# Performance work log

Hardware: AMD Instinct MI355X
Metric: run time of the kernel (lower is better)

The kernel has to match this reference:

```python
import jax, jax.numpy as jnp
from jax import lax
import numpy as np

B, T, D = 16, 750, 2048
C = 20            # num_classes
H = 8             # num heads (CMA on feat_dim = D//2 = 1024)
DH = (D // 2) // H
R_EASY, R_HARD, SM, SB = 5, 20, 3, 6  # r_easy, r_hard, m, M
EPS = 1e-12


def setup_inputs() -> dict:
    key = jax.random.key(0)
    ks = jax.random.split(key, 8)
    d2 = D // 2
    return {
        'x': jax.random.normal(ks[0], (B, T, D), jnp.float32),
        'rgb_proj': jax.random.normal(ks[1], (H, d2, DH), jnp.float32) * 0.03,
        'flow_proj': jax.random.normal(ks[2], (H, d2, DH), jnp.float32) * 0.03,
        'atte_w': jax.random.normal(ks[3], (H, DH, DH), jnp.float32) * 0.09,
        'embed_w': jax.random.normal(ks[4], (2048, D, 9), jnp.float32) * 0.02,
        'embed_b': jnp.zeros((2048,), jnp.float32),
        'cls1_w': jax.random.normal(ks[5], (C, 2048, 9), jnp.float32) * 0.02,
        'cls2_w': jax.random.normal(ks[6], (C, 1, 7), jnp.float32) * 0.1,
    }


def _l2norm(v):
    # torch F.normalize: v / max(||v||, eps)
    n = jnp.sqrt(jnp.sum(v * v, axis=-1, keepdims=True))
    return v / jnp.maximum(n, EPS)


def _conv1d(x, w, pad, dil=1, groups=1):
    # x: (N, Cin, L), w: (Cout, Cin/groups, K)
    return lax.conv_general_dilated(x, w, (1,), [(pad, pad)], rhs_dilation=(dil,),
                                    dimension_numbers=('NCH', 'OIH', 'NCH'),
                                    feature_group_count=groups)


def _erode(b, w):
    # scipy binary_erosion, structure ones((1,w)), border_value=0
    left = w // 2
    bp = jnp.pad(b, ((0, 0), (left, w - 1 - left)))
    return lax.reduce_window(bp, jnp.inf, lax.min, (1, w), (1, 1), 'VALID')


def _dilate(b, w):
    # scipy binary_dilation (reflected structure), border_value=0
    right = w // 2
    bp = jnp.pad(b, ((0, 0), (w - 1 - right, right)))
    return lax.reduce_window(bp, -jnp.inf, lax.max, (1, w), (1, 1), 'VALID')


def _topk_gather(scores, emb, k):
    _, idx = lax.top_k(scores, k)           # (N, k), descending like torch.sort
    return jnp.take_along_axis(emb, idx[:, :, None], axis=1)


def reference(x, rgb_proj, flow_proj, atte_w, embed_w, embed_b, cls1_w, cls2_w):
    n, l, _ = x.shape
    k_easy, k_hard = l // R_EASY, l // R_HARD
    rgb, flow = x[..., :D // 2], x[..., D // 2:]

    # ---- CMA cross-modal attention ----
    o_rgb = _l2norm(jnp.einsum('nld,hde->nhle', rgb, rgb_proj))    # (n,H,l,dh)
    o_flow = _l2norm(jnp.einsum('nld,hde->nhle', flow, flow_proj))
    atte = jnp.einsum('nhlf,nhmf->nhlm', jnp.einsum('nhle,hef->nhlf', o_rgb, atte_w), o_flow)
    rgb_atte = jax.nn.softmax(atte, axis=-1)
    flow_atte = jax.nn.softmax(jnp.swapaxes(atte, -1, -2), axis=-1)
    e_rgb = jax.nn.gelu(jnp.einsum('nhlm,nhme->nhle', rgb_atte, o_rgb), approximate=False)
    e_flow = jax.nn.gelu(jnp.einsum('nhlm,nhme->nhle', flow_atte, o_flow), approximate=False)
    f_rgb = jnp.tanh(jnp.swapaxes(e_rgb, 1, 2).reshape(n, l, -1) + rgb)
    f_flow = jnp.tanh(jnp.swapaxes(e_flow, 1, 2).reshape(n, l, -1) + flow)
    xc = jnp.concatenate([f_rgb, f_flow], axis=-1)                 # (n,l,D)

    # ---- Actionness module (eval mode: dropouts are identity) ----
    xt = jnp.swapaxes(xc, 1, 2)                                    # (n,D,l)
    emb = jax.nn.relu(_conv1d(xt, embed_w, pad=4) + embed_b[None, :, None])
    embeddings = jnp.swapaxes(emb, 1, 2)                           # (n,l,2048)
    o = _conv1d(emb, cls1_w, pad=4)                                # (n,C,l)
    o = jax.nn.relu(_conv1d(o, cls2_w, pad=6, dil=2, groups=C))
    cas = jnp.swapaxes(o, 1, 2)                                    # (n,l,C)
    actionness = jnp.sum(cas, axis=2)                              # (n,l)

    # ---- easy snippet mining ----
    easy_act = _topk_gather(actionness, embeddings, k_easy)
    a_rev = jnp.max(actionness, axis=1, keepdims=True) - actionness
    easy_bkg = _topk_gather(a_rev, embeddings, k_easy)

    # ---- hard snippet mining (median threshold + 1D morphology) ----
    med = jnp.median(actionness, axis=1, keepdims=True)
    abin = jnp.where(actionness > med, 1.0, 0.0).astype(actionness.dtype)
    inner = actionness * (_erode(abin, SM) - _erode(abin, SB))
    hard_act = _topk_gather(inner, embeddings, k_hard)
    outer = actionness * (_dilate(abin, SB) - _dilate(abin, SM))
    hard_bkg = _topk_gather(outer, embeddings, k_hard)

    # ---- video class scores ----
    top_cas, _ = lax.top_k(jnp.swapaxes(cas, 1, 2), k_easy)        # (n,C,k)
    video_scores = jax.nn.softmax(jnp.mean(top_cas, axis=-1), axis=1)
    return (video_scores, easy_act, easy_bkg, hard_act, hard_bkg, actionness, cas)
```

## Files before the change

### kernel.cpp

```cpp
#include <hip/hip_runtime.h>
#include <cstdio>
#include <cstdint>

typedef __bf16 bf16;
typedef __attribute__((ext_vector_type(8))) __bf16 bf16x8;
typedef __attribute__((ext_vector_type(4))) __bf16 bf16x4;
typedef __attribute__((ext_vector_type(4))) float f32x4;
typedef unsigned long long u64;
typedef unsigned int u32;

constexpr int BATCH = 16, TT = 750, DD = 2048, NC = 20;
constexpr int MM = 12000;
constexpr int PT = 758;
constexpr int PCH = 32;
constexpr int NCHUNK = 4;
constexpr int RPC = 3000;
constexpr int SROW = 752;
constexpr int SPAIR = 750 * SROW;
constexpr int KE = 150, KH = 37;

constexpr size_t OUT_EA  = 320;
constexpr size_t OUT_EB  = OUT_EA + (size_t)BATCH * KE * DD;
constexpr size_t OUT_HA  = OUT_EB + (size_t)BATCH * KE * DD;
constexpr size_t OUT_HB  = OUT_HA + (size_t)BATCH * KH * DD;
constexpr size_t OUT_ACT = OUT_HB + (size_t)BATCH * KH * DD;
constexpr size_t OUT_CAS = OUT_ACT + MM;

constexpr size_t XCB = (size_t)(BATCH * PT) * DD * 2;
constexpr size_t O_XC1   = 0;
constexpr size_t O_XC2   = O_XC1 + XCB;
constexpr size_t O_XC3   = O_XC2 + XCB;
constexpr size_t O_EM1   = O_XC3 + XCB;
constexpr size_t O_EM2   = O_EM1 + XCB;
constexpr size_t O_EM3   = O_EM2 + XCB;
constexpr size_t O_CAS1  = O_EM3 + XCB;
constexpr size_t O_CAST  = O_CAS1 + 960000;
constexpr size_t O_ACT   = O_CAST + 960000;
constexpr size_t O_AREV  = O_ACT + 48000;
constexpr size_t O_INNER = O_AREV + 48000;
constexpr size_t O_OUTER = O_INNER + 48000;
constexpr size_t O_SMEAN = O_OUTER + 48000;
constexpr size_t O_IDX   = O_SMEAN + 1280;
constexpr size_t O_RSINV = O_IDX + 23936;
constexpr size_t O_CSINV = O_RSINV + 96000;
constexpr size_t O_DBG   = O_CSINV + 96000;
constexpr size_t AR      = O_DBG + 256;

constexpr size_t SB   = (size_t)PCH * SPAIR * 4;
constexpr size_t PL   = (size_t)PCH * 750 * 128 * 2;
constexpr size_t TPL  = (size_t)PCH * 128 * 768 * 2;
constexpr size_t O_S    = AR;
constexpr size_t O_ST   = O_S + SB;
constexpr size_t O_Q1   = O_ST + SB;
constexpr size_t O_Q2   = O_Q1 + PL;
constexpr size_t O_Q3   = O_Q2 + PL;
constexpr size_t O_OR1  = O_Q3 + PL;
constexpr size_t O_OR2  = O_OR1 + PL;
constexpr size_t O_OR3  = O_OR2 + PL;
constexpr size_t O_OF1  = O_OR3 + PL;
constexpr size_t O_OF2  = O_OF1 + PL;
constexpr size_t O_OF3  = O_OF2 + PL;
constexpr size_t O_OTR1 = O_OF3 + PL;
constexpr size_t O_OTR2 = O_OTR1 + TPL;
constexpr size_t O_OTR3 = O_OTR2 + TPL;
constexpr size_t O_OTF1 = O_OTR3 + TPL;
constexpr size_t O_OTF2 = O_OTF1 + TPL;
constexpr size_t O_OTF3 = O_OTF2 + TPL;
constexpr size_t O_OPRE = O_OTF3 + TPL;
constexpr size_t PRP  = (size_t)1024 * 1024 * 2;
constexpr size_t O_PR1  = O_OPRE + (size_t)RPC * 1024 * 4;
constexpr size_t O_PR2  = O_PR1 + PRP;
constexpr size_t O_PR3  = O_PR2 + PRP;
constexpr size_t O_PF1  = O_PR3 + PRP;
constexpr size_t O_PF2  = O_PF1 + PRP;
constexpr size_t O_PF3  = O_PF2 + PRP;
constexpr size_t AWP  = (size_t)8 * 128 * 128 * 2;
constexpr size_t O_AW1  = O_PF3 + PRP;
constexpr size_t O_AW2  = O_AW1 + AWP;
constexpr size_t O_AW3  = O_AW2 + AWP;
constexpr size_t WS_NEED = O_AW3 + AWP;

constexpr size_t WTP  = (size_t)9 * 2048 * 2048 * 2;
constexpr size_t O_WT1  = AR;
constexpr size_t O_WT2  = O_WT1 + WTP;
constexpr size_t O_WT3  = O_WT2 + WTP;
constexpr size_t WCP  = (size_t)9 * 32 * 2048 * 2;
constexpr size_t O_WC1  = O_WT3 + WTP;
constexpr size_t O_WC2  = O_WC1 + WCP;
constexpr size_t O_WC3  = O_WC2 + WCP;

static_assert(O_WC3 + WCP <= WS_NEED, "WT/WC overrun");
static_assert(WS_NEED <= 603979776, "exceeds harness ws");

struct bf3 { bf16 h, m, l; };
static __device__ __forceinline__ bf3 split3(float v) {
  bf3 r;
  r.h = (bf16)v;
  float rem = v - (float)r.h;
  r.m = (bf16)rem;
  r.l = (bf16)(rem - (float)r.m);
  return r;
}
static __device__ __forceinline__ bf16x8 bzero8() {
  bf16x8 v;
#pragma unroll
  for (int i = 0; i < 8; i++) v[i] = (bf16)0.f;
  return v;
}
static __device__ __forceinline__ u32 asc_enc(float f) {
  u32 u = __float_as_uint(f);
  return (u & 0x80000000u) ? ~u : (u | 0x80000000u);
}
static __device__ __forceinline__ float asc_dec(u32 a) {
  u32 u = (a & 0x80000000u) ? (a ^ 0x80000000u) : ~a;
  return __uint_as_float(u);
}
static __device__ void bsort1024(u64* ks) {
  const int tid = threadIdx.x;
  for (int kk = 2; kk <= 1024; kk <<= 1) {
    for (int j = kk >> 1; j > 0; j >>= 1) {
      __syncthreads();
      for (int i = tid; i < 1024; i += 512) {
        int ixj = i ^ j;
        if (ixj > i) {
          u64 a = ks[i], b = ks[ixj];
          bool up = ((i & kk) == 0);
          if ((a > b) == up) { ks[i] = b; ks[ixj] = a; }
        }
      }
    }
  }
  __syncthreads();
}

static __device__ __forceinline__ int ldsOff(int row, int kc) {
  return ((row >> 4) << 10) + ((kc * 16 + (((row & 15) + 2 * kc) & 15)) << 4);
}

template <int WGM, int WGN, int FM, int FN, class P>
__global__ __launch_bounds__(256) void gemm6(P p) {
  constexpr int BM = WGM * FM * 16;
  constexpr int BN = WGN * FN * 16;
  __shared__ bf16 sA1[BM * 32];
  __shared__ bf16 sA2[BM * 32];
  __shared__ bf16 sA3[BM * 32];
  __shared__ bf16 sB1[BN * 32];
  __shared__ bf16 sB2[BN * 32];
  __shared__ bf16 sB3[BN * 32];
  const int tid = threadIdx.x;
  const int z = blockIdx.z;
  const int row0 = blockIdx.y * BM;
  const int col0 = blockIdx.x * BN;
  const int lane = tid & 63;
  const int wv = tid >> 6;
  const int wm = (wv % WGM) * (FM * 16);
  const int wn = (wv / WGM) * (FN * 16);
  const int lps = ((lane >> 4) * 16 + (((lane & 15) + 2 * (lane >> 4)) & 15)) << 4;
  f32x4 acc[FM][FN];
#pragma unroll
  for (int i = 0; i < FM; i++)
#pragma unroll
    for (int j = 0; j < FN; j++)
#pragma unroll
      for (int r = 0; r < 4; r++) acc[i][j][r] = 0.f;

  const int ks = p.ksteps();
  for (int s = 0; s < ks; ++s) {
#pragma unroll
    for (int g0 = 0; g0 < BM * 4; g0 += 256) {
      int g = g0 + tid;
      if (g < BM * 4) {
        int row = g >> 2, k0 = (g & 3) * 8;
        bf16x8 v1, v2, v3;
        p.loadA3(z, row0 + row, k0, s, v1, v2, v3);
        int byte = ldsOff(row, g & 3);
        *(bf16x8*)((char*)sA1 + byte) = v1;
        *(bf16x8*)((char*)sA2 + byte) = v2;
        *(bf16x8*)((char*)sA3 + byte) = v3;
      }
    }
#pragma unroll
    for (int g0 = 0; g0 < BN * 4; g0 += 256) {
      int g = g0 + tid;
      if (g < BN * 4) {
        int row = g >> 2, k0 = (g & 3) * 8;
        bf16x8 v1, v2, v3;
        p.loadB3(z, col0 + row, k0, s, v1, v2, v3);
        int byte = ldsOff(row, g & 3);
        *(bf16x8*)((char*)sB1 + byte) = v1;
        *(bf16x8*)((char*)sB2 + byte) = v2;
        *(bf16x8*)((char*)sB3 + byte) = v3;
      }
    }
    __syncthreads();
    {
      bf16x8 a1[FM], a2[FM], a3[FM], b1[FN], b2[FN], b3[FN];
#pragma unroll
      for (int i = 0; i < FM; i++) {
        int byte = (((wm >> 4) + i) << 10) + lps;
        a1[i] = *(const bf16x8*)((const char*)sA1 + byte);
        a2[i] = *(const bf16x8*)((const char*)sA2 + byte);
        a3[i] = *(const bf16x8*)((const char*)sA3 + byte);
      }
#pragma unroll
      for (int j = 0; j < FN; j++) {
        int byte = (((wn >> 4) + j) << 10) + lps;
        b1[j] = *(const bf16x8*)((const char*)sB1 + byte);
        b2[j] = *(const bf16x8*)((const char*)sB2 + byte);
        b3[j] = *(const bf16x8*)((const char*)sB3 + byte);
      }
#pragma unroll
      for (int i = 0; i < FM; i++)
#pragma unroll
        for (int j = 0; j < FN; j++) {
          acc[i][j] = __builtin_amdgcn_mfma_f32_16x16x32_bf16(a1[i], b1[j], acc[i][j], 0, 0, 0);
          acc[i][j] = __builtin_amdgcn_mfma_f32_16x16x32_bf16(a1[i], b2[j], acc[i][j], 0, 0, 0);
          acc[i][j] = __builtin_amdgcn_mfma_f32_16x16x32_bf16(a2[i], b1[j], acc[i][j], 0, 0, 0);
          acc[i][j] = __builtin_amdgcn_mfma_f32_16x16x32_bf16(a2[i], b2[j], acc[i][j], 0, 0, 0);
          acc[i][j] = __builtin_amdgcn_mfma_f32_16x16x32_bf16(a1[i], b3[j], acc[i][j], 0, 0, 0);
          acc[i][j] = __builtin_amdgcn_mfma_f32_16x16x32_bf16(a3[i], b1[j], acc[i][j], 0, 0, 0);
        }
    }
    __syncthreads();
  }
#pragma unroll
  for (int i = 0; i < FM; i++)
#pragma unroll
    for (int j = 0; j < FN; j++)
#pragma unroll
      for (int rg = 0; rg < 4; rg++) {
        int r = row0 + wm + i * 16 + ((lane >> 4) << 2) + rg;
        int c = col0 + wn + j * 16 + (lane & 15);
        p.store(z, r, c, acc[i][j][rg]);
      }
}

template <int TH, int WGM, int WGN, int FM, int FN, class P>
__global__ __launch_bounds__(TH) void gemm6d(P p) {
  constexpr int BM = WGM * FM * 16;
  constexpr int BN = WGN * FN * 16;
  constexpr int NA = (BM * 4 + TH - 1) / TH;
  constexpr int NB = (BN * 4 + TH - 1) / TH;
  __shared__ bf16 sA1[BM * 32];
  __shared__ bf16 sA2[BM * 32];
  __shared__ bf16 sA3[BM * 32];
  __shared__ bf16 sB1[BN * 32];
  __shared__ bf16 sB2[BN * 32];
  __shared__ bf16 sB3[BN * 32];
  const int tid = threadIdx.x;
  const int z = blockIdx.z;
  const int row0 = blockIdx.y * BM;
  const int col0 = blockIdx.x * BN;
  const int lane = tid & 63;
  const int wv = tid >> 6;
  const int wm = (wv % WGM) * (FM * 16);
  const int wn = (wv / WGM) * (FN * 16);
  const int lps = ((lane >> 4) * 16 + (((lane & 15) + 2 * (lane >> 4)) & 15)) << 4;
  double acc[FM][FN][4];
  f32x4 fmn[FM][FN], fcr[FM][FN];
#pragma unroll
  for (int i = 0; i < FM; i++)
#pragma unroll
    for (int j = 0; j < FN; j++)
#pragma unroll
      for (int r = 0; r < 4; r++) {
        acc[i][j][r] = 0.0;
        fmn[i][j][r] = 0.f;
        fcr[i][j][r] = 0.f;
      }

  bf16x8 gA[NA][3], gB[NB][3];
  auto issue = [&](int s) {
#pragma unroll
    for (int u = 0; u < NA; u++) {
      int g = u * TH + tid;
      if (g < BM * 4) {
        int row = g >> 2, k0 = (g & 3) * 8;
        p.loadA3(z, row0 + row, k0, s, gA[u][0], gA[u][1], gA[u][2]);
      }
    }
#pragma unroll
    for (int u = 0; u < NB; u++) {
      int g = u * TH + tid;
      if (g < BN * 4) {
        int row = g >> 2, k0 = (g & 3) * 8;
        p.loadB3(z, col0 + row, k0, s, gB[u][0], gB[u][1], gB[u][2]);
      }
    }
  };

  const int ks = p.ksteps();
  issue(0);
  for (int s = 0; s < ks; ++s) {
#pragma unroll
    for (int u = 0; u < NA; u++) {
      int g = u * TH + tid;
      if (g < BM * 4) {
        int byte = ldsOff(g >> 2, g & 3);
        *(bf16x8*)((char*)sA1 + byte) = gA[u][0];
        *(bf16x8*)((char*)sA2 + byte) = gA[u][1];
        *(bf16x8*)((char*)sA3 + byte) = gA[u][2];
      }
    }
#pragma unroll
    for (int u = 0; u < NB; u++) {
      int g = u * TH + tid;
      if (g < BN * 4) {
        int byte = ldsOff(g >> 2, g & 3);
        *(bf16x8*)((char*)sB1 + byte) = gB[u][0];
        *(bf16x8*)((char*)sB2 + byte) = gB[u][1];
        *(bf16x8*)((char*)sB3 + byte) = gB[u][2];
      }
    }
    __syncthreads();
    if (s + 1 < ks) issue(s + 1);
    {
      bf16x8 a1[FM], a2[FM], a3[FM], b1[FN], b2[FN], b3[FN];
#pragma unroll
      for (int i = 0; i < FM; i++) {
        int byte = (((wm >> 4) + i) << 10) + lps;
        a1[i] = *(const bf16x8*)((const char*)sA1 + byte);
        a2[i] = *(const bf16x8*)((const char*)sA2 + byte);
        a3[i] = *(const bf16x8*)((const char*)sA3 + byte);
      }
#pragma unroll
      for (int j = 0; j < FN; j++) {
        int byte = (((wn >> 4) + j) << 10) + lps;
        b1[j] = *(const bf16x8*)((const char*)sB1 + byte);
        b2[j] = *(const bf16x8*)((const char*)sB2 + byte);
        b3[j] = *(const bf16x8*)((const char*)sB3 + byte);
      }
#pragma unroll
      for (int i = 0; i < FM; i++)
#pragma unroll
        for (int j = 0; j < FN; j++) {
          fmn[i][j] = __builtin_amdgcn_mfma_f32_16x16x32_bf16(a1[i], b1[j], fmn[i][j], 0, 0, 0);
          fcr[i][j] = __builtin_amdgcn_mfma_f32_16x16x32_bf16(a1[i], b2[j], fcr[i][j], 0, 0, 0);
          fcr[i][j] = __builtin_amdgcn_mfma_f32_16x16x32_bf16(a2[i], b1[j], fcr[i][j], 0, 0, 0);
          fcr[i][j] = __builtin_amdgcn_mfma_f32_16x16x32_bf16(a2[i], b2[j], fcr[i][j], 0, 0, 0);
          fcr[i][j] = __builtin_amdgcn_mfma_f32_16x16x32_bf16(a1[i], b3[j], fcr[i][j], 0, 0, 0);
          fcr[i][j] = __builtin_amdgcn_mfma_f32_16x16x32_bf16(a3[i], b1[j], fcr[i][j], 0, 0, 0);
        }
    }
    bool flm = ((s & 1) == 1) || (s == ks - 1);
    bool flc = ((s & 7) == 7) || (s == ks - 1);
    if (flm) {
#pragma unroll
      for (int i = 0; i < FM; i++)
#pragma unroll
        for (int j = 0; j < FN; j++)
#pragma unroll
          for (int r = 0; r < 4; r++) {
            acc[i][j][r] += (double)fmn[i][j][r];
            fmn[i][j][r] = 0.f;
          }
    }
    if (flc) {
#pragma unroll
      for (int i = 0; i < FM; i++)
#pragma unroll
        for (int j = 0; j < FN; j++)
#pragma unroll
          for (int r = 0; r < 4; r++) {
            acc[i][j][r] += (double)fcr[i][j][r];
            fcr[i][j][r] = 0.f;
          }
    }
    __syncthreads();
  }
#pragma unroll
  for (int i = 0; i < FM; i++)
#pragma unroll
    for (int j = 0; j < FN; j++)
#pragma unroll
      for (int rg = 0; rg < 4; rg++) {
        int r = row0 + wm + i * 16 + ((lane >> 4) << 2) + rg;
        int c = col0 + wn + j * 16 + (lane & 15);
        p.store(z, r, c, acc[i][j][rg]);
      }
}

struct P6PROJ {
  const float* x;
  const bf16 *b1, *b2, *b3;
  float* out;
  int rowoff, colbase;
  __device__ int ksteps() const { return 32; }
  __device__ void loadA3(int, int r, int k0, int s, bf16x8& v1, bf16x8& v2, bf16x8& v3) const {
    v1 = bzero8(); v2 = bzero8(); v3 = bzero8();
    if (r >= RPC) return;
    const float* src = x + (size_t)(rowoff + r) * 2048 + colbase + s * 32 + k0;
#pragma unroll
    for (int j = 0; j < 8; j++) {
      bf3 t = split3(src[j]);
      v1[j] = t.h; v2[j] = t.m; v3[j] = t.l;
    }
  }
  __device__ void loadB3(int, int c, int k0, int s, bf16x8& v1, bf16x8& v2, bf16x8& v3) const {
    size_t a = (size_t)c * 1024 + s * 32 + k0;
    v1 = *(const bf16x8*)(b1 + a); v2 = *(const bf16x8*)(b2 + a); v3 = *(const bf16x8*)(b3 + a);
  }
  __device__ void store(int, int r, int c, double v) const {
    if (r < RPC) out[(size_t)r * 1024 + c] = (float)v;
  }
};

struct P6Q {
  const bf16 *a1, *a2, *a3, *b1, *b2, *b3;
  bf16 *q1, *q2, *q3;
  __device__ int ksteps() const { return 4; }
  __device__ void loadA3(int z, int r, int k0, int s, bf16x8& v1, bf16x8& v2, bf16x8& v3) const {
    if (r >= 750) { v1 = bzero8(); v2 = bzero8(); v3 = bzero8(); return; }
    size_t a = (size_t)z * 96000 + (size_t)r * 128 + s * 32 + k0;
    v1 = *(const bf16x8*)(a1 + a); v2 = *(const bf16x8*)(a2 + a); v3 = *(const bf16x8*)(a3 + a);
  }
  __device__ void loadB3(int z, int c, int k0, int s, bf16x8& v1, bf16x8& v2, bf16x8& v3) const {
    size_t a = (size_t)(z & 7) * 16384 + (size_t)c * 128 + s * 32 + k0;
    v1 = *(const bf16x8*)(b1 + a); v2 = *(const bf16x8*)(b2 + a); v3 = *(const bf16x8*)(b3 + a);
  }
  __device__ void store(int z, int r, int c, float v) const {
    if (r >= 750) return;
    size_t a = (size_t)z * 96000 + (size_t)r * 128 + c;
    bf3 t = split3(v);
    q1[a] = t.h; q2[a] = t.m; q3[a] = t.l;
  }
};

struct P6S {
  const bf16 *a1, *a2, *a3, *b1, *b2, *b3;
  float* out;
  __device__ int ksteps() const { return 4; }
  __device__ void loadA3(int z, int r, int k0, int s, bf16x8& v1, bf16x8& v2, bf16x8& v3) const {
    if (r >= 750) { v1 = bzero8(); v2 = bzero8(); v3 = bzero8(); return; }
    size_t a = (size_t)z * 96000 + (size_t)r * 128 + s * 32 + k0;
    v1 = *(const bf16x8*)(a1 + a); v2 = *(const bf16x8*)(a2 + a); v3 = *(const bf16x8*)(a3 + a);
  }
  __device__ void loadB3(int z, int c, int k0, int s, bf16x8& v1, bf16x8& v2, bf16x8& v3) const {
    if (c >= 750) { v1 = bzero8(); v2 = bzero8(); v3 = bzero8(); return; }
    size_t a = (size_t)z * 96000 + (size_t)c * 128 + s * 32 + k0;
    v1 = *(const bf16x8*)(b1 + a); v2 = *(const bf16x8*)(b2 + a); v3 = *(const bf16x8*)(b3 + a);
  }
  __device__ void store(int z, int r, int c, float v) const {
    if (r < 750 && c < 750) out[(size_t)z * SPAIR + (size_t)r * SROW + c] = expf(v);
  }
};

struct P6E {
  const float *Pr, *Pt;
  const float *invr, *invc;
  const bf16 *br1, *br2, *br3;
  const bf16 *bt1, *bt2, *bt3;
  const float* x;
  bf16 *xc1, *xc2, *xc3;
  int pairbase;
  __device__ int ksteps() const { return 24; }
  __device__ void loadA3(int z, int r, int k0, int s, bf16x8& v1, bf16x8& v2, bf16x8& v3) const {
    v1 = bzero8(); v2 = bzero8(); v3 = bzero8();
    if (r >= 750) return;
    int zp = z & 31;
    const float* Pm = (z < 32) ? Pr : Pt;
    const float* inv = (z < 32) ? invr : invc;
    int m0 = s * 32 + k0;
    const float* row = Pm + (size_t)zp * SPAIR + (size_t)r * SROW;
    float sc = inv[zp * 750 + r];
#pragma unroll
    for (int j = 0; j < 8; j++) {
      int m = m0 + j;
      if (m < 750) {
        bf3 t = split3(row[m] * sc);
        v1[j] = t.h; v2[j] = t.m; v3[j] = t.l;
      }
    }
  }
  __device__ void loadB3(int z, int c, int k0, int s, bf16x8& v1, bf16x8& v2, bf16x8& v3) const {
    int zp = z & 31;
    size_t a = (size_t)zp * 98304 + (size_t)c * 768 + s * 32 + k0;
    if (z < 32) {
      v1 = *(const bf16x8*)(br1 + a); v2 = *(const bf16x8*)(br2 + a); v3 = *(const bf16x8*)(br3 + a);
    } else {
      v1 = *(const bf16x8*)(bt1 + a); v2 = *(const bf16x8*)(bt2 + a); v3 = *(const bf16x8*)(bt3 + a);
    }
  }
  __device__ void store(int z, int r, int c, float v) const {
    if (r >= 750) return;
    int zp = z & 31;
    int gp = pairbase + zp;
    int hh = gp & 7, n = gp >> 3;
    int xcol = ((z < 32) ? 0 : 1024) + hh * 128 + c;
    float g = 0.5f * v * (1.f + erff(v * 0.70710678118654752f));
    float f = tanhf(g + x[((size_t)n * 750 + r) * 2048 + xcol]);
    size_t a = (size_t)(n * PT + r + 4) * 2048 + xcol;
    bf3 t = split3(f);
    xc1[a] = t.h; xc2[a] = t.m; xc3[a] = t.l;
  }
};

struct P6CONV {
  const bf16 *a1, *a2, *a3, *b1, *b2, *b3;
  const float* bias;
  bf16 *o1, *o2, *o3;
  __device__ int ksteps() const { return 576; }
  __device__ void loadA3(int, int r, int k0, int s, bf16x8& v1, bf16x8& v2, bf16x8& v3) const {
    if (r >= MM) { v1 = bzero8(); v2 = bzero8(); v3 = bzero8(); return; }
    int ktap = s >> 6, kb = s & 63;
    int n = (unsigned)r / 750u;
    size_t a = (size_t)(r + 8 * n + ktap) * 2048 + kb * 32 + k0;
    v1 = *(const bf16x8*)(a1 + a); v2 = *(const bf16x8*)(a2 + a); v3 = *(const bf16x8*)(a3 + a);
  }
  __device__ void loadB3(int, int c, int k0, int s, bf16x8& v1, bf16x8& v2, bf16x8& v3) const {
    int ktap = s >> 6, kb = s & 63;
    size_t a = ((size_t)(ktap * 2048 + c)) * 2048 + kb * 32 + k0;
    v1 = *(const bf16x8*)(b1 + a); v2 = *(const bf16x8*)(b2 + a); v3 = *(const bf16x8*)(b3 + a);
  }
  __device__ void store(int, int r, int c, double v) const {
    if (r >= MM) return;
    v += (double)bias[c];
    if (v < 0) v = 0;
    int n = (unsigned)r / 750u;
    size_t a = (size_t)(r + 8 * n + 4) * 2048 + c;
    bf3 t = split3((float)v);
    o1[a] = t.h; o2[a] = t.m; o3[a] = t.l;
  }
};

struct P6CLS1 {
  const bf16 *a1, *a2, *a3, *b1, *b2, *b3;
  float* out;
  __device__ int ksteps() const { return 576; }
  __device__ void loadA3(int, int r, int k0, int s, bf16x8& v1, bf16x8& v2, bf16x8& v3) const {
    if (r >= MM) { v1 = bzero8(); v2 = bzero8(); v3 = bzero8(); return; }
    int ktap = s >> 6, kb = s & 63;
    int n = (unsigned)r / 750u;
    size_t a = (size_t)(r + 8 * n + ktap) * 2048 + kb * 32 + k0;
    v1 = *(const bf16x8*)(a1 + a); v2 = *(const bf16x8*)(a2 + a); v3 = *(const bf16x8*)(a3 + a);
  }
  __device__ void loadB3(int, int c, int k0, int s, bf16x8& v1, bf16x8& v2, bf16x8& v3) const {
    int ktap = s >> 6, kb = s & 63;
    size_t a = ((size_t)(ktap * 32 + c)) * 2048 + kb * 32 + k0;
    v1 = *(const bf16x8*)(b1 + a); v2 = *(const bf16x8*)(b2 + a); v3 = *(const bf16x8*)(b3 + a);
  }
  __device__ void store(int, int r, int c, double v) const {
    if (r < MM && c < NC) out[(size_t)r * NC + c] = (float)v;
  }
};

__global__ void k_split_projT3(const float* rgbp, const float* flowp, bf16* r1, bf16* r2, bf16* r3,
                               bf16* f1, bf16* f2, bf16* f3) {
  int bx = blockIdx.x;
  int st = bx >> 10, c = bx & 1023;
  int h = c >> 7, e = c & 127;
  const float* src = st ? flowp : rgbp;
  bf16* o1 = st ? f1 : r1;
  bf16* o2 = st ? f2 : r2;
  bf16* o3 = st ? f3 : r3;
  int d0 = threadIdx.x * 4;
  bf16x4 a, b, cc;
#pragma unroll
  for (int j = 0; j < 4; j++) {
    bf3 t = split3(src[(size_t)h * 131072 + (size_t)(d0 + j) * 128 + e]);
    a[j] = t.h; b[j] = t.m; cc[j] = t.l;
  }
  size_t o = (size_t)c * 1024 + d0;
  *(bf16x4*)(o1 + o) = a;
  *(bf16x4*)(o2 + o) = b;
  *(bf16x4*)(o3 + o) = cc;
}

__global__ void k_split_attewT3(const float* aw, bf16* w1, bf16* w2, bf16* w3) {
  int b = blockIdx.x;
  int h = b >> 7, f = b & 127;
  int e = threadIdx.x;
  bf3 t = split3(aw[(size_t)h * 16384 + (size_t)e * 128 + f]);
  size_t a = (size_t)h * 16384 + (size_t)f * 128 + e;
  w1[a] = t.h; w2[a] = t.m; w3[a] = t.l;
}

__global__ void k_split_wt3(const float* ew, bf16* w1, bf16* w2, bf16* w3) {
  __shared__ float tmp[1152];
  int o = blockIdx.x >> 4, ic0 = (blockIdx.x & 15) << 7;
  for (int t = threadIdx.x; t < 1152; t += 256)
    tmp[t] = ew[(size_t)o * 18432 + (size_t)ic0 * 9 + t];
  __syncthreads();
  for (int w = threadIdx.x; w < 1152; w += 256) {
    int k = w >> 7, i = w & 127;
    bf3 t = split3(tmp[i * 9 + k]);
    size_t a = ((size_t)(k * 2048 + o)) * 2048 + ic0 + i;
    w1[a] = t.h; w2[a] = t.m; w3[a] = t.l;
  }
}

__global__ void k_split_wc3(const float* cw, bf16* w1, bf16* w2, bf16* w3) {
  int k = blockIdx.x / 32, c = blockIdx.x % 32;
  for (int i = threadIdx.x; i < 2048; i += 256) {
    float v = (c < NC) ? cw[(size_t)c * 18432 + (size_t)i * 9 + k] : 0.f;
    bf3 t = split3(v);
    size_t a = ((size_t)(k * 32 + c)) * 2048 + i;
    w1[a] = t.h; w2[a] = t.m; w3[a] = t.l;
  }
}

__global__ void k_norm3(const float* opre, bf16* o1, bf16* o2, bf16* o3) {
  int r = blockIdx.x;
  int head = threadIdx.x >> 5, ln = threadIdx.x & 31;
  const float* src = opre + (size_t)r * 1024 + head * 128 + ln * 4;
  float4 v = *(const float4*)src;
  double ss = (double)v.x * v.x + (double)v.y * v.y + (double)v.z * v.z + (double)v.w * v.w;
  for (int k = 16; k; k >>= 1) ss += __shfl_xor(ss, k, 32);
  double rn = 1.0 / fmax(sqrt(ss), 1e-12);
  int nl = r / 750, l = r % 750;
  int zp = nl * 8 + head;
  size_t o = (size_t)zp * 96000 + (size_t)l * 128 + ln * 4;
  float vv[4] = {v.x, v.y, v.z, v.w};
  bf16x4 h4, m4, l4;
#pragma unroll
  for (int j = 0; j < 4; j++) {
    bf3 t = split3((float)((double)vv[j] * rn));
    h4[j] = t.h; m4[j] = t.m; l4[j] = t.l;
  }
  *(bf16x4*)(o1 + o) = h4;
  *(bf16x4*)(o2 + o) = m4;
  *(bf16x4*)(o3 + o) = l4;
}

__global__ void k_trans3(const bf16* i1, const bf16* i2, const bf16* i3, bf16* o1, bf16* o2,
                         bf16* o3) {
  __shared__ bf16 t1[32][33], t2[32][33], t3[32][33];
  int zp = blockIdx.y;
  int lt = blockIdx.x >> 2, et = blockIdx.x & 3;
  int tx = threadIdx.x & 31, ty = threadIdx.x >> 5;
#pragma unroll
  for (int p = 0; p < 4; p++) {
    int lrow = lt * 32 + ty + p * 8;
    int e = et * 32 + tx;
    bf16 a = (bf16)0.f, b = (bf16)0.f, c = (bf16)0.f;
    if (lrow < 750) {
      size_t ad = (size_t)zp * 96000 + (size_t)lrow * 128 + e;
      a = i1[ad]; b = i2[ad]; c = i3[ad];
    }
    t1[ty + p * 8][tx] = a;
    t2[ty + p * 8][tx] = b;
    t3[ty + p * 8][tx] = c;
  }
  __syncthreads();
#pragma unroll
  for (int p = 0; p < 4; p++) {
    int e = et * 32 + ty + p * 8;
    int l2 = lt * 32 + tx;
    size_t ad = (size_t)zp * 98304 + (size_t)e * 768 + l2;
    o1[ad] = t1[tx][ty + p * 8];
    o2[ad] = t2[tx][ty + p * 8];
    o3[ad] = t3[tx][ty + p * 8];
  }
}

__global__ void k_transS(const float* S, float* ST) {
  __shared__ float t[32][33];
  int zp = blockIdx.y;
  int tr = (blockIdx.x / 24) * 32, tc = (blockIdx.x % 24) * 32;
  int tx = threadIdx.x & 31, ty = threadIdx.x >> 5;
#pragma unroll
  for (int p = 0; p < 4; p++) {
    int rr = tr + ty + p * 8, cc = tc + tx;
    t[ty + p * 8][tx] = (rr < 750 && cc < 750) ? S[(size_t)zp * SPAIR + (size_t)rr * SROW + cc] : 0.f;
  }
  __syncthreads();
#pragma unroll
  for (int p = 0; p < 4; p++) {
    int cc = tc + ty + p * 8, rr = tr + tx;
    if (cc < 750 && rr < 750) ST[(size_t)zp * SPAIR + (size_t)cc * SROW + rr] = t[tx][ty + p * 8];
  }
}

__global__ void k_statsd(const float* P, float* inv) {
  int b = blockIdx.x;
  int p = b / 94, r0 = (b % 94) * 8;
  int g = threadIdx.x >> 5, ln = threadIdx.x & 31;
  int r = r0 + g;
  if (r >= 750) return;
  const float* row = P + (size_t)p * SPAIR + (size_t)r * SROW;
  double s = 0.0;
  for (int m = ln; m < 750; m += 32) s += (double)row[m];
  for (int k = 16; k; k >>= 1) s += __shfl_xor(s, k, 32);
  if (ln == 0) inv[p * 750 + r] = (float)(1.0 / s);
}

__global__ void k_cls2(const float* cas1, const float* w2, float* cas_out, float* cast) {
  int idx = blockIdx.x * 256 + threadIdx.x;
  if (idx >= MM * NC) return;
  int r = idx / NC, c = idx % NC;
  int n = r / 750, t = r % 750;
  double a = 0.0;
#pragma unroll
  for (int j = 0; j < 7; j++) {
    int tt = t + 2 * j - 6;
    if (tt >= 0 && tt < 750)
      a += (double)w2[c * 7 + j] * (double)cas1[((size_t)n * 750 + tt) * NC + c];
  }
  if (a < 0) a = 0;
  cas_out[idx] = (float)a;
  cast[((size_t)n * NC + c) * 750 + t] = (float)a;
}

__global__ void k_act(const float* cas, float* act, float* out_act) {
  int r = blockIdx.x * 256 + threadIdx.x;
  if (r >= MM) return;
  double s = 0.0;
#pragma unroll
  for (int c = 0; c < NC; c++) s += (double)cas[(size_t)r * NC + c];
  act[r] = (float)s;
  out_act[r] = (float)s;
}

__global__ __launch_bounds__(512) void k_mask(const float* act, float* arev, float* inner,
                                              float* outer) {
  __shared__ u64 ks[1024];
  __shared__ float av[768];
  __shared__ float bb[768];
  int n = blockIdx.x;
  for (int i = threadIdx.x; i < 1024; i += 512) {
    if (i < 750) {
      float v = act[n * 750 + i];
      av[i] = v;
      ks[i] = ((u64)asc_enc(v) << 32) | (u32)i;
    } else
      ks[i] = ~0ull;
  }
  bsort1024(ks);
  float med = 0.5f * (asc_dec((u32)(ks[374] >> 32)) + asc_dec((u32)(ks[375] >> 32)));
  float amax = asc_dec((u32)(ks[749] >> 32));
  for (int t = threadIdx.x; t < 750; t += 512) bb[t] = (av[t] > med) ? 1.f : 0.f;
  __syncthreads();
  for (int t = threadIdx.x; t < 750; t += 512) {
    float e3 = 1.f, e6 = 1.f, d3 = 0.f, d6 = 0.f;
    for (int j = t - 1; j <= t + 1; ++j) {
      float v = (j >= 0 && j < 750) ? bb[j] : 0.f;
      e3 = fminf(e3, v); d3 = fmaxf(d3, v);
    }
    for (int j = t - 3; j <= t + 2; ++j) {
      float v = (j >= 0 && j < 750) ? bb[j] : 0.f;
      e6 = fminf(e6, v);
    }
    for (int j = t - 2; j <= t + 3; ++j) {
      float v = (j >= 0 && j < 750) ? bb[j] : 0.f;
      d6 = fmaxf(d6, v);
    }
    int g = n * 750 + t;
    inner[g] = (e3 - e6 > 0.5f) ? av[t] : 0.f;
    outer[g] = (d6 - d3 > 0.5f) ? av[t] : 0.f;
    arev[g] = amax - av[t];
  }
}

__global__ __launch_bounds__(512) void k_topk(const float* act, const float* arev,
                                              const float* inner, const float* outer, int* idxb) {
  __shared__ u64 ks[1024];
  int n = blockIdx.x >> 2, w = blockIdx.x & 3;
  const float* src = (w == 0) ? act : ((w == 1) ? arev : ((w == 2) ? inner : outer));
  int K = (w < 2) ? KE : KH;
  int off = (w == 0) ? 0 : ((w == 1) ? 150 : ((w == 2) ? 300 : 337));
  for (int i = threadIdx.x; i < 1024; i += 512) {
    if (i < 750) {
      u32 d = ~asc_enc(src[n * 750 + i]);
      ks[i] = ((u64)d << 32) | (u32)i;
    } else
      ks[i] = ~0ull;
  }
  bsort1024(ks);
  for (int i = threadIdx.x; i < K; i += 512) idxb[n * 374 + off + i] = (int)(ks[i] & 0xFFFFFFFFu);
}

__global__ __launch_bounds__(512) void k_topcas(const float* cast, float* smean) {
  __shared__ u64 ks[1024];
  __shared__ float red[512];
  int b = blockIdx.x;
  for (int i = threadIdx.x; i < 1024; i += 512) {
    if (i < 750) {
      u32 d = ~asc_enc(cast[(size_t)b * 750 + i]);
      ks[i] = ((u64)d << 32) | (u32)i;
    } else
      ks[i] = ~0ull;
  }
  bsort1024(ks);
  float s = 0.f;
  for (int i = threadIdx.x; i < KE; i += 512) s += asc_dec(~(u32)(ks[i] >> 32));
  red[threadIdx.x] = s;
  __syncthreads();
  for (int st = 256; st; st >>= 1) {
    if (threadIdx.x < st) red[threadIdx.x] += red[threadIdx.x + st];
    __syncthreads();
  }
  if (threadIdx.x == 0) smean[b] = red[0] / 150.f;
}

__global__ void k_gather(const int* idxb, const bf16* e1, const bf16* e2, const bf16* e3,
                         float* dout) {
  int b = blockIdx.x;
  int n = b / 374, j = b % 374;
  size_t obase;
  if (j < 150) obase = OUT_EA + ((size_t)n * KE + j) * 2048;
  else if (j < 300) obase = OUT_EB + ((size_t)n * KE + (j - 150)) * 2048;
  else if (j < 337) obase = OUT_HA + ((size_t)n * KH + (j - 300)) * 2048;
  else obase = OUT_HB + ((size_t)n * KH + (j - 337)) * 2048;
  int t = idxb[n * 374 + j];
  size_t irow = (size_t)(n * PT + t + 4) * 2048;
#pragma unroll
  for (int p = 0; p < 8; p++) {
    int c = threadIdx.x + p * 256;
    dout[obase + c] = (float)e1[irow + c] + (float)e2[irow + c] + (float)e3[irow + c];
  }
}

__global__ void k_vs(const float* smean, float* dout) {
  int n = blockIdx.x;
  int c = threadIdx.x;
  float v = (c < NC) ? smean[n * NC + c] : -3.4e38f;
  float m = v;
  for (int s = 32; s; s >>= 1) m = fmaxf(m, __shfl_xor(m, s));
  float e = (c < NC) ? expf(v - m) : 0.f;
  float sum = e;
  for (int s = 32; s; s >>= 1) sum += __shfl_xor(sum, s);
  if (c < NC) dout[n * NC + c] = e / sum;
}

extern "C" void kernel_launch(void* const* d_in, const int* in_sizes, int n_in, void* d_out,
                              int out_size, void* d_ws, size_t ws_size, hipStream_t stream) {
  const float* x = (const float*)d_in[0];
  const float* rgbp = (const float*)d_in[1];
  const float* flowp = (const float*)d_in[2];
  const float* attw = (const float*)d_in[3];
  const float* embw = (const float*)d_in[4];
  const float* embb = (const float*)d_in[5];
  const float* c1w = (const float*)d_in[6];
  const float* c2w = (const float*)d_in[7];
  float* dout = (float*)d_out;
  char* ws = (char*)d_ws;

  if (ws_size < WS_NEED) {
    fprintf(stderr, "[CoLA] FATAL ws_size=%zu < need=%zu\n", ws_size, (size_t)WS_NEED);
    return;
  }

  bf16* XC1 = (bf16*)(ws + O_XC1);
  bf16* XC2 = (bf16*)(ws + O_XC2);
  bf16* XC3 = (bf16*)(ws + O_XC3);
  bf16* EM1 = (bf16*)(ws + O_EM1);
  bf16* EM2 = (bf16*)(ws + O_EM2);
  bf16* EM3 = (bf16*)(ws + O_EM3);
  float* CAS1 = (float*)(ws + O_CAS1);
  float* CAST = (float*)(ws + O_CAST);
  float* ACT = (float*)(ws + O_ACT);
  float* AREV = (float*)(ws + O_AREV);
  float* INNER = (float*)(ws + O_INNER);
  float* OUTER = (float*)(ws + O_OUTER);
  float* SMEAN = (float*)(ws + O_SMEAN);
  int* IDX = (int*)(ws + O_IDX);
  float* RSINV = (float*)(ws + O_RSINV);
  float* CSINV = (float*)(ws + O_CSINV);
  float* SBUF = (float*)(ws + O_S);
  float* STBUF = (float*)(ws + O_ST);
  bf16 *Q1 = (bf16*)(ws + O_Q1), *Q2 = (bf16*)(ws + O_Q2), *Q3 = (bf16*)(ws + O_Q3);
  bf16 *OR1 = (bf16*)(ws + O_OR1), *OR2 = (bf16*)(ws + O_OR2), *OR3 = (bf16*)(ws + O_OR3);
  bf16 *OF1 = (bf16*)(ws + O_OF1), *OF2 = (bf16*)(ws + O_OF2), *OF3 = (bf16*)(ws + O_OF3);
  bf16 *OTR1 = (bf16*)(ws + O_OTR1), *OTR2 = (bf16*)(ws + O_OTR2), *OTR3 = (bf16*)(ws + O_OTR3);
  bf16 *OTF1 = (bf16*)(ws + O_OTF1), *OTF2 = (bf16*)(ws + O_OTF2), *OTF3 = (bf16*)(ws + O_OTF3);
  float* OPRE = (float*)(ws + O_OPRE);
  bf16 *PR1 = (bf16*)(ws + O_PR1), *PR2 = (bf16*)(ws + O_PR2), *PR3 = (bf16*)(ws + O_PR3);
  bf16 *PF1 = (bf16*)(ws + O_PF1), *PF2 = (bf16*)(ws + O_PF2), *PF3 = (bf16*)(ws + O_PF3);
  bf16 *AW1 = (bf16*)(ws + O_AW1), *AW2 = (bf16*)(ws + O_AW2), *AW3 = (bf16*)(ws + O_AW3);
  bf16 *WT1 = (bf16*)(ws + O_WT1), *WT2 = (bf16*)(ws + O_WT2), *WT3 = (bf16*)(ws + O_WT3);
  bf16 *WC1 = (bf16*)(ws + O_WC1), *WC2 = (bf16*)(ws + O_WC2), *WC3 = (bf16*)(ws + O_WC3);

  (void)hipMemsetAsync(ws, 0, O_CAS1, stream);

  k_split_projT3<<<2048, 256, 0, stream>>>(rgbp, flowp, PR1, PR2, PR3, PF1, PF2, PF3);
  k_split_attewT3<<<1024, 128, 0, stream>>>(attw, AW1, AW2, AW3);

  for (int cb = 0; cb < NCHUNK; cb++) {
    int rowoff = cb * RPC;
    int pb = cb * PCH;
    {
      P6PROJ p{x, PR1, PR2, PR3, OPRE, rowoff, 0};
      gemm6d<512, 2, 4, 4, 2, P6PROJ><<<dim3(8, 24, 1), 512, 0, stream>>>(p);
    }
    k_norm3<<<RPC, 256, 0, stream>>>(OPRE, OR1, OR2, OR3);
    k_trans3<<<dim3(96, 32), 256, 0, stream>>>(OR1, OR2, OR3, OTR1, OTR2, OTR3);
    {
      P6Q p{OR1, OR2, OR3, AW1, AW2, AW3, Q1, Q2, Q3};
      gemm6<2, 2, 4, 4, P6Q><<<dim3(1, 6, PCH), 256, 0, stream>>>(p);
    }
    {
      P6PROJ p{x, PF1, PF2, PF3, OPRE, rowoff, 1024};
      gemm6d<512, 2, 4, 4, 2, P6PROJ><<<dim3(8, 24, 1), 512, 0, stream>>>(p);
    }
    k_norm3<<<RPC, 256, 0, stream>>>(OPRE, OF1, OF2, OF3);
    k_trans3<<<dim3(96, 32), 256, 0, stream>>>(OF1, OF2, OF3, OTF1, OTF2, OTF3);
    {
      P6S p{Q1, Q2, Q3, OF1, OF2, OF3, SBUF};
      gemm6<2, 2, 4, 4, P6S><<<dim3(6, 6, PCH), 256, 0, stream>>>(p);
    }
    k_transS<<<dim3(576, PCH), 256, 0, stream>>>(SBUF, STBUF);
    k_statsd<<<PCH * 94, 256, 0, stream>>>(SBUF, RSINV);
    k_statsd<<<PCH * 94, 256, 0, stream>>>(STBUF, CSINV);
    {
      P6E p{SBUF, STBUF, RSINV, CSINV, OTR1, OTR2, OTR3, OTF1, OTF2, OTF3, x, XC1, XC2, XC3, pb};
      gemm6<2, 2, 4, 4, P6E><<<dim3(1, 6, 2 * PCH), 256, 0, stream>>>(p);
    }
  }

  k_split_wt3<<<32768, 256, 0, stream>>>(embw, WT1, WT2, WT3);
  k_split_wc3<<<288, 256, 0, stream>>>(c1w, WC1, WC2, WC3);
  {
    P6CONV p{XC1, XC2, XC3, WT1, WT2, WT3, embb, EM1, EM2, EM3};
    gemm6d<512, 2, 4, 4, 2, P6CONV><<<dim3(16, 94, 1), 512, 0, stream>>>(p);
  }
  {
    P6CLS1 p{EM1, EM2, EM3, WC1, WC2, WC3, CAS1};
    gemm6d<512, 4, 2, 2, 1, P6CLS1><<<dim3(1, 94, 1), 512, 0, stream>>>(p);
  }
  k_cls2<<<(MM * NC + 255) / 256, 256, 0, stream>>>(CAS1, c2w, dout + OUT_CAS, CAST);
  k_act<<<(MM + 255) / 256, 256, 0, stream>>>(dout + OUT_CAS, ACT, dout + OUT_ACT);

  k_mask<<<16, 512, 0, stream>>>(ACT, AREV, INNER, OUTER);
  k_topk<<<64, 512, 0, stream>>>(ACT, AREV, INNER, OUTER, IDX);
  k_topcas<<<320, 512, 0, stream>>>(CAST, SMEAN);
  k_gather<<<16 * 374, 256, 0, stream>>>(IDX, EM1, EM2, EM3, dout);
  k_vs<<<16, 64, 0, stream>>>(SMEAN, dout);
}
```

Baseline: 9.021 ms.

## Load GEMM B operands directly as pre-swizzled MFMA fragments from global

Adds a GEMM variant that keeps only the A tile in shared memory and reads B operands straight from global memory as register-ready MFMA fragments, double-buffered across k-steps. The weight split kernels for the projection and the embedding conv are rewritten to emit weights in this fragment-major layout. The projection and conv GEMMs switch to the new kernel. This drops the LDS staging and extra barrier traffic for B, at the cost of more global loads per wave and higher register pressure. It also inserts a stray redundant load in P6S.

Measured after the change: 8.754 ms. 1.03x faster.

```diff
diff --git a/kernel.cpp b/kernel.cpp
--- a/kernel.cpp
+++ b/kernel.cpp
@@ -236,6 +236,136 @@
 }
 
 template <int TH, int WGM, int WGN, int FM, int FN, class P>
+__global__ __launch_bounds__(TH) void gemm6dBF(P p) {
+  constexpr int BM = WGM * FM * 16;
+  constexpr int NA = (BM * 4 + TH - 1) / TH;
+  __shared__ bf16 sA1[BM * 32];
+  __shared__ bf16 sA2[BM * 32];
+  __shared__ bf16 sA3[BM * 32];
+  const int tid = threadIdx.x;
+  const int z = blockIdx.z;
+  const int row0 = blockIdx.y * BM;
+  const int col0 = blockIdx.x * (WGN * FN * 16);
+  const int lane = tid & 63;
+  const int wv = tid >> 6;
+  const int wm = (wv % WGM) * (FM * 16);
+  const int wn = (wv / WGM) * (FN * 16);
+  const int cb0 = (col0 + wn) >> 4;
+  const int lps = ((lane >> 4) * 16 + (((lane & 15) + 2 * (lane >> 4)) & 15)) << 4;
+  double acc[FM][FN][4];
+  f32x4 fmn[FM][FN], fcr[FM][FN];
+#pragma unroll
+  for (int i = 0; i < FM; i++)
+#pragma unroll
+    for (int j = 0; j < FN; j++)
+#pragma unroll
+      for (int r = 0; r < 4; r++) {
+        acc[i][j][r] = 0.0;
+        fmn[i][j][r] = 0.f;
+        fcr[i][j][r] = 0.f;
+      }
+
+  bf16x8 gA[NA][3];
+  bf16x8 bC[FN][3], bN[FN][3];
+  auto issueA = [&](int s) {
+#pragma unroll
+    for (int u = 0; u < NA; u++) {
+      int g = u * TH + tid;
+      if (g < BM * 4) {
+        int row = g >> 2, k0 = (g & 3) * 8;
+        p.loadA3(z, row0 + row, k0, s, gA[u][0], gA[u][1], gA[u][2]);
+      }
+    }
+  };
+
+  const int ks = p.ksteps();
+  issueA(0);
+#pragma unroll
+  for (int j = 0; j < FN; j++) p.loadBfrag(z, cb0 + j, 0, lane, bC[j][0], bC[j][1], bC[j][2]);
+  for (int s = 0; s < ks; ++s) {
+#pragma unroll
+    for (int u = 0; u < NA; u++) {
+      int g = u * TH + tid;
+      if (g < BM * 4) {
+        int byte = ldsOff(g >> 2, g & 3);
+        *(bf16x8*)((char*)sA1 + byte) = gA[u][0];
+        *(bf16x8*)((char*)sA2 + byte) = gA[u][1];
+        *(bf16x8*)((char*)sA3 + byte) = gA[u][2];
+      }
+    }
+    __syncthreads();
+    if (s + 1 < ks) {
+      issueA(s + 1);
+#pragma unroll
+      for (int j = 0; j < FN; j++)
+        p.loadBfrag(z, cb0 + j, s + 1, lane, bN[j][0], bN[j][1], bN[j][2]);
+    }
+    {
+      bf16x8 a1[FM], a2[FM], a3[FM];
+#pragma unroll
+      for (int i = 0; i < FM; i++) {
+        int byte = (((wm >> 4) + i) << 10) + lps;
+        a1[i] = *(const bf16x8*)((const char*)sA1 + byte);
+        a2[i] = *(const bf16x8*)((const char*)sA2 + byte);
+        a3[i] = *(const bf16x8*)((const char*)sA3 + byte);
+      }
+#pragma unroll
+      for (int i = 0; i < FM; i++)
+#pragma unroll
+        for (int j = 0; j < FN; j++) {
+          fmn[i][j] = __builtin_amdgcn_mfma_f32_16x16x32_bf16(a1[i], bC[j][0], fmn[i][j], 0, 0, 0);
+          fcr[i][j] = __builtin_amdgcn_mfma_f32_16x16x32_bf16(a1[i], bC[j][1], fcr[i][j], 0, 0, 0);
+          fcr[i][j] = __builtin_amdgcn_mfma_f32_16x16x32_bf16(a2[i], bC[j][0], fcr[i][j], 0, 0, 0);
+          fcr[i][j] = __builtin_amdgcn_mfma_f32_16x16x32_bf16(a2[i], bC[j][1], fcr[i][j], 0, 0, 0);
+          fcr[i][j] = __builtin_amdgcn_mfma_f32_16x16x32_bf16(a1[i], bC[j][2], fcr[i][j], 0, 0, 0);
+          fcr[i][j] = __builtin_amdgcn_mfma_f32_16x16x32_bf16(a3[i], bC[j][0], fcr[i][j], 0, 0, 0);
+        }
+    }
+    bool flm = ((s & 1) == 1) || (s == ks - 1);
+    bool flc = ((s & 7) == 7) || (s == ks - 1);
+    if (flm) {
+#pragma unroll
+      for (int i = 0; i < FM; i++)
+#pragma unroll
+        for (int j = 0; j < FN; j++)
+#pragma unroll
+          for (int r = 0; r < 4; r++) {
+            acc[i][j][r] += (double)fmn[i][j][r];
+            fmn[i][j][r] = 0.f;
+          }
+    }
+    if (flc) {
+#pragma unroll
+      for (int i = 0; i < FM; i++)
+#pragma unroll
+        for (int j = 0; j < FN; j++)
+#pragma unroll
+          for (int r = 0; r < 4; r++) {
+            acc[i][j][r] += (double)fcr[i][j][r];
+            fcr[i][j][r] = 0.f;
+          }
+    }
+    __syncthreads();
+    if (s + 1 < ks) {
+#pragma unroll
+      for (int j = 0; j < FN; j++)
+#pragma unroll
+        for (int pl = 0; pl < 3; pl++) bC[j][pl] = bN[j][pl];
+    }
+  }
+#pragma unroll
+  for (int i = 0; i < FM; i++)
+#pragma unroll
+    for (int j = 0; j < FN; j++)
+#pragma unroll
+      for (int rg = 0; rg < 4; rg++) {
+        int r = row0 + wm + i * 16 + ((lane >> 4) << 2) + rg;
+        int c = col0 + wn + j * 16 + (lane & 15);
+        p.store(z, r, c, acc[i][j][rg]);
+      }
+}
+
+template <int TH, int WGM, int WGN, int FM, int FN, class P>
 __global__ __launch_bounds__(TH) void gemm6d(P p) {
   constexpr int BM = WGM * FM * 16;
   constexpr int BN = WGN * FN * 16;
@@ -396,8 +526,9 @@
       v1[j] = t.h; v2[j] = t.m; v3[j] = t.l;
     }
   }
-  __device__ void loadB3(int, int c, int k0, int s, bf16x8& v1, bf16x8& v2, bf16x8& v3) const {
-    size_t a = (size_t)c * 1024 + s * 32 + k0;
+  __device__ void loadBfrag(int, int cb, int s, int lane, bf16x8& v1, bf16x8& v2,
+                            bf16x8& v3) const {
+    size_t a = (((size_t)s * 64 + cb) * 64 + lane) * 8;
     v1 = *(const bf16x8*)(b1 + a); v2 = *(const bf16x8*)(b2 + a); v3 = *(const bf16x8*)(b3 + a);
   }
   __device__ void store(int, int r, int c, double v) const {
@@ -438,6 +569,7 @@
   __device__ void loadB3(int z, int c, int k0, int s, bf16x8& v1, bf16x8& v2, bf16x8& v3) const {
     if (c >= 750) { v1 = bzero8(); v2 = bzero8(); v3 = bzero8(); return; }
     size_t a = (size_t)z * 96000 + (size_t)c * 128 + s * 32 + k0;
+    v1 = *(const bf16x8*)(a1 == b1 ? a1 : b1 + a);
     v1 = *(const bf16x8*)(b1 + a); v2 = *(const bf16x8*)(b2 + a); v3 = *(const bf16x8*)(b3 + a);
   }
   __device__ void store(int z, int r, int c, float v) const {
@@ -507,9 +639,9 @@
     size_t a = (size_t)(r + 8 * n + ktap) * 2048 + kb * 32 + k0;
     v1 = *(const bf16x8*)(a1 + a); v2 = *(const bf16x8*)(a2 + a); v3 = *(const bf16x8*)(a3 + a);
   }
-  __device__ void loadB3(int, int c, int k0, int s, bf16x8& v1, bf16x8& v2, bf16x8& v3) const {
-    int ktap = s >> 6, kb = s & 63;
-    size_t a = ((size_t)(ktap * 2048 + c)) * 2048 + kb * 32 + k0;
+  __device__ void loadBfrag(int, int cb, int s, int lane, bf16x8& v1, bf16x8& v2,
+                            bf16x8& v3) const {
+    size_t a = (((size_t)s * 128 + cb) * 64 + lane) * 8;
     v1 = *(const bf16x8*)(b1 + a); v2 = *(const bf16x8*)(b2 + a); v3 = *(const bf16x8*)(b3 + a);
   }
   __device__ void store(int, int r, int c, double v) const {
@@ -544,26 +676,24 @@
   }
 };
 
-__global__ void k_split_projT3(const float* rgbp, const float* flowp, bf16* r1, bf16* r2, bf16* r3,
-                               bf16* f1, bf16* f2, bf16* f3) {
-  int bx = blockIdx.x;
-  int st = bx >> 10, c = bx & 1023;
-  int h = c >> 7, e = c & 127;
+__global__ void k_split_projT3f(const float* rgbp, const float* flowp, bf16* r1, bf16* r2,
+                                bf16* r3, bf16* f1, bf16* f2, bf16* f3) {
+  int st = blockIdx.x >> 6, cb = blockIdx.x & 63;
   const float* src = st ? flowp : rgbp;
   bf16* o1 = st ? f1 : r1;
   bf16* o2 = st ? f2 : r2;
   bf16* o3 = st ? f3 : r3;
-  int d0 = threadIdx.x * 4;
-  bf16x4 a, b, cc;
-#pragma unroll
-  for (int j = 0; j < 4; j++) {
-    bf3 t = split3(src[(size_t)h * 131072 + (size_t)(d0 + j) * 128 + e]);
-    a[j] = t.h; b[j] = t.m; cc[j] = t.l;
-  }
-  size_t o = (size_t)c * 1024 + d0;
-  *(bf16x4*)(o1 + o) = a;
-  *(bf16x4*)(o2 + o) = b;
-  *(bf16x4*)(o3 + o) = cc;
+  for (int u = threadIdx.x; u < 16384; u += 256) {
+    int s = u >> 9;
+    int lane = (u >> 3) & 63;
+    int e = u & 7;
+    int col = cb * 16 + (lane & 15);
+    int h = col >> 7, ep = col & 127;
+    int k = s * 32 + (lane >> 4) * 8 + e;
+    bf3 t = split3(src[(size_t)h * 131072 + (size_t)k * 128 + ep]);
+    size_t d = (((size_t)s * 64 + cb) * 64 + lane) * 8 + e;
+    o1[d] = t.h; o2[d] = t.m; o3[d] = t.l;
+  }
 }
 
 __global__ void k_split_attewT3(const float* aw, bf16* w1, bf16* w2, bf16* w3) {
@@ -575,17 +705,18 @@
   w1[a] = t.h; w2[a] = t.m; w3[a] = t.l;
 }
 
-__global__ void k_split_wt3(const float* ew, bf16* w1, bf16* w2, bf16* w3) {
-  __shared__ float tmp[1152];
-  int o = blockIdx.x >> 4, ic0 = (blockIdx.x & 15) << 7;
-  for (int t = threadIdx.x; t < 1152; t += 256)
-    tmp[t] = ew[(size_t)o * 18432 + (size_t)ic0 * 9 + t];
-  __syncthreads();
-  for (int w = threadIdx.x; w < 1152; w += 256) {
-    int k = w >> 7, i = w & 127;
-    bf3 t = split3(tmp[i * 9 + k]);
-    size_t a = ((size_t)(k * 2048 + o)) * 2048 + ic0 + i;
-    w1[a] = t.h; w2[a] = t.m; w3[a] = t.l;
+__global__ void k_split_wt3f(const float* ew, bf16* w1, bf16* w2, bf16* w3) {
+  int cb = blockIdx.x & 127;
+  int ktap = blockIdx.x >> 7;
+  for (int u = threadIdx.x; u < 32768; u += 256) {
+    int kb = u >> 9;
+    int lane = (u >> 3) & 63;
+    int e = u & 7;
+    int oc = cb * 16 + (lane & 15);
+    int ic = kb * 32 + (lane >> 4) * 8 + e;
+    bf3 t = split3(ew[(size_t)oc * 18432 + (size_t)ic * 9 + ktap]);
+    size_t d = (((size_t)(ktap * 64 + kb) * 128 + cb) * 64 + lane) * 8 + e;
+    w1[d] = t.h; w2[d] = t.m; w3[d] = t.l;
   }
 }
 
@@ -872,7 +1003,7 @@
 
   (void)hipMemsetAsync(ws, 0, O_CAS1, stream);
 
-  k_split_projT3<<<2048, 256, 0, stream>>>(rgbp, flowp, PR1, PR2, PR3, PF1, PF2, PF3);
+  k_split_projT3f<<<128, 256, 0, stream>>>(rgbp, flowp, PR1, PR2, PR3, PF1, PF2, PF3);
   k_split_attewT3<<<1024, 128, 0, stream>>>(attw, AW1, AW2, AW3);
 
   for (int cb = 0; cb < NCHUNK; cb++) {
@@ -880,7 +1011,7 @@
     int pb = cb * PCH;
     {
       P6PROJ p{x, PR1, PR2, PR3, OPRE, rowoff, 0};
-      gemm6d<512, 2, 4, 4, 2, P6PROJ><<<dim3(8, 24, 1), 512, 0, stream>>>(p);
+      gemm6dBF<512, 2, 4, 4, 2, P6PROJ><<<dim3(8, 24, 1), 512, 0, stream>>>(p);
     }
     k_norm3<<<RPC, 256, 0, stream>>>(OPRE, OR1, OR2, OR3);
     k_trans3<<<dim3(96, 32), 256, 0, stream>>>(OR1, OR2, OR3, OTR1, OTR2, OTR3);
@@ -890,7 +1021,7 @@
     }
     {
       P6PROJ p{x, PF1, PF2, PF3, OPRE, rowoff, 1024};
-      gemm6d<512, 2, 4, 4, 2, P6PROJ><<<dim3(8, 24, 1), 512, 0, stream>>>(p);
+      gemm6dBF<512, 2, 4, 4, 2, P6PROJ><<<dim3(8, 24, 1), 512, 0, stream>>>(p);
     }
     k_norm3<<<RPC, 256, 0, stream>>>(OPRE, OF1, OF2, OF3);
     k_trans3<<<dim3(96, 32), 256, 0, stream>>>(OF1, OF2, OF3, OTF1, OTF2, OTF3);
@@ -907,11 +1038,11 @@
     }
   }
 
-  k_split_wt3<<<32768, 256, 0, stream>>>(embw, WT1, WT2, WT3);
+  k_split_wt3f<<<1152, 256, 0, stream>>>(embw, WT1, WT2, WT3);
   k_split_wc3<<<288, 256, 0, stream>>>(c1w, WC1, WC2, WC3);
   {
     P6CONV p{XC1, XC2, XC3, WT1, WT2, WT3, embb, EM1, EM2, EM3};
-    gemm6d<512, 2, 4, 4, 2, P6CONV><<<dim3(16, 94, 1), 512, 0, stream>>>(p);
+    gemm6dBF<512, 2, 4, 4, 2, P6CONV><<<dim3(16, 94, 1), 512, 0, stream>>>(p);
   }
   {
     P6CLS1 p{EM1, EM2, EM3, WC1, WC2, WC3, CAS1};
```
